# Kernel optimization log

Measured on AMD Instinct MI355X. Metric: run time of the kernel, lower is better.

Reference implementation:

```python
import jax, jax.numpy as jnp
import numpy as np

N = 250_000        # nodes
E = 8_000_000      # directed edges
F_IN = 16          # dataset.num_features
H = 8              # latent_dim
G = 512            # number of graphs in the batch


def setup_inputs() -> dict:
    key = jax.random.key(0)
    k = jax.random.split(key, 9)
    x = jax.random.normal(k[0], (N, F_IN), dtype=jnp.float32)
    edge_index = jax.random.randint(k[1], (2, E), 0, N, dtype=jnp.int64)
    batch = jnp.sort(jax.random.randint(k[2], (N,), 0, G, dtype=jnp.int64))
    W1 = jax.random.normal(k[3], (F_IN, H), dtype=jnp.float32) * 0.25
    b1 = jax.random.normal(k[4], (H,), dtype=jnp.float32) * 0.1
    W2 = jax.random.normal(k[5], (H, H), dtype=jnp.float32) * 0.35
    b2 = jax.random.normal(k[6], (H,), dtype=jnp.float32) * 0.1
    Wl = jax.random.normal(k[7], (H, 1), dtype=jnp.float32) * 0.35
    bl = jax.random.normal(k[8], (1,), dtype=jnp.float32) * 0.1
    return {"x": x, "edge_index": edge_index, "batch": batch,
            "W1": W1, "b1": b1, "W2": W2, "b2": b2, "Wl": Wl, "bl": bl}


def _gcn_conv(x, src, dst, deg_inv_sqrt, W, b, num_nodes):
    # PyG GCNConv (default): h = x @ W ; msg = norm * h[src] ; scatter-add to dst ; + bias
    h = x @ W                                    # [N, H]
    norm = deg_inv_sqrt[src] * deg_inv_sqrt[dst]  # [E+N]
    msgs = h[src] * norm[:, None]                 # [E+N, H]
    out = jax.ops.segment_sum(msgs, dst, num_segments=num_nodes)
    return out + b


def reference(x, edge_index, batch, W1, b1, W2, b2, Wl, bl):
    num_nodes = x.shape[0]
    loops = jnp.arange(num_nodes, dtype=edge_index.dtype)
    src = jnp.concatenate([edge_index[0], loops])  # self-loops appended
    dst = jnp.concatenate([edge_index[1], loops])
    # symmetric normalization: deg over destination (incl. self-loops)
    deg = jax.ops.segment_sum(jnp.ones_like(dst, dtype=x.dtype), dst,
                              num_segments=num_nodes)
    dis = jnp.where(deg > 0, jax.lax.rsqrt(jnp.maximum(deg, 1.0)), 0.0)
    h = jax.nn.relu(_gcn_conv(x, src, dst, dis, W1, b1, num_nodes))
    h = jax.nn.relu(_gcn_conv(h, src, dst, dis, W2, b2, num_nodes))
    pooled = jax.ops.segment_sum(h, batch, num_segments=G)  # global_add_pool -> [G, H]
    return jax.nn.sigmoid(pooled @ Wl + bl)                 # [G, 1]
```

## Files before the change

### kernel.cpp

```cpp
#include <hip/hip_runtime.h>
#include <math.h>

#define BLK 256
#define CH 4096
#define NBMAX 1024


__global__ void k_init0(int* __restrict__ ghist, float* __restrict__ zacc,
                        int* __restrict__ rowptr, int nb, int ng, int n, int E,
                        int primary) {
  int i = blockIdx.x * BLK + threadIdx.x;
  if (i < nb) ghist[i] = 0;
  if (i < ng) zacc[i] = 0.f;
  if (primary && i == 0) rowptr[n] = E;
}

__global__ void k_hist(const int* __restrict__ dst, int* __restrict__ ghist,
                       int E, int nb, int chunk) {
  __shared__ int h[NBMAX];
  for (int i = threadIdx.x; i < NBMAX; i += BLK) h[i] = 0;
  __syncthreads();
  long long s0 = (long long)blockIdx.x * chunk;
  int c = (int)min((long long)chunk, (long long)E - s0);
  if (c == chunk && (chunk & 3) == 0) {
    const int4* d4 = (const int4*)(dst + s0);
    int m = chunk >> 2;
    for (int i = threadIdx.x; i < m; i += BLK) {
      int4 v = d4[i];
      atomicAdd(&h[v.x >> 8], 1); atomicAdd(&h[v.y >> 8], 1);
      atomicAdd(&h[v.z >> 8], 1); atomicAdd(&h[v.w >> 8], 1);
    }
  } else {
    for (int i = threadIdx.x; i < c; i += BLK)
      atomicAdd(&h[dst[s0 + i] >> 8], 1);
  }
  __syncthreads();
  for (int b = threadIdx.x; b < nb; b += BLK)
    if (h[b]) atomicAdd(&ghist[b], h[b]);
}

__global__ void k_scan(const int* __restrict__ ghist, int* __restrict__ base,
                       int* __restrict__ cursor, int nb, int E) {
  __shared__ int temp[BLK];
  int t = threadIdx.x;
  int v[4]; int sm = 0;
  #pragma unroll
  for (int k = 0; k < 4; ++k) {
    int idx = t * 4 + k;
    v[k] = (idx < nb) ? ghist[idx] : 0;
    sm += v[k];
  }
  temp[t] = sm; __syncthreads();
  int inc = sm;
  for (int off = 1; off < BLK; off <<= 1) {
    int u = (t >= off) ? temp[t - off] : 0; __syncthreads();
    inc += u; temp[t] = inc; __syncthreads();
  }
  int run = inc - sm;
  #pragma unroll
  for (int k = 0; k < 4; ++k) {
    int idx = t * 4 + k;
    if (idx < nb) { base[idx] = run; cursor[idx] = run; }
    run += v[k];
  }
  if (t == BLK - 1) base[nb] = E;
}

__global__ void k_bin(const int* __restrict__ src, const int* __restrict__ dst,
                      int* __restrict__ cursor, int* __restrict__ binned,
                      int E, int nb) {
  __shared__ int cb[NBMAX + 1];
  __shared__ int cur[NBMAX];
  __shared__ int gofs[NBMAX];
  __shared__ int temp[BLK];
  __shared__ int stage[CH];
  __shared__ unsigned short bkt[CH];
  int t = threadIdx.x;
  for (int i = t; i < NBMAX; i += BLK) { cb[i] = 0; cur[i] = 0; }
  __syncthreads();
  long long s0 = (long long)blockIdx.x * CH;
  int c = (int)min((long long)CH, (long long)E - s0);
  if (c == CH) {
    const int4* d4 = (const int4*)(dst + s0);
    for (int i = t; i < (CH >> 2); i += BLK) {
      int4 v = d4[i];
      atomicAdd(&cb[v.x >> 8], 1); atomicAdd(&cb[v.y >> 8], 1);
      atomicAdd(&cb[v.z >> 8], 1); atomicAdd(&cb[v.w >> 8], 1);
    }
  } else {
    for (int i = t; i < c; i += BLK) atomicAdd(&cb[dst[s0 + i] >> 8], 1);
  }
  __syncthreads();
  int v[4];
  #pragma unroll
  for (int k = 0; k < 4; ++k) v[k] = cb[t * 4 + k];
  int sm = v[0] + v[1] + v[2] + v[3];
  temp[t] = sm; __syncthreads();
  int inc = sm;
  for (int off = 1; off < BLK; off <<= 1) {
    int u = (t >= off) ? temp[t - off] : 0; __syncthreads();
    inc += u; temp[t] = inc; __syncthreads();
  }
  #pragma unroll
  for (int k = 0; k < 4; ++k) {
    int b = t * 4 + k;
    if (v[k]) gofs[b] = atomicAdd(&cursor[b], v[k]);
  }
  int run = inc - sm;
  #pragma unroll
  for (int k = 0; k < 4; ++k) { cb[t * 4 + k] = run; run += v[k]; }
  if (t == BLK - 1) cb[NBMAX] = c;
  __syncthreads();
  #pragma unroll
  for (int k = 0; k < 4; ++k) {
    int b = t * 4 + k;
    int s_ = cb[b], e_ = cb[b + 1];
    if (e_ > s_) {
      gofs[b] -= s_;
      for (int i = s_; i < e_; ++i) bkt[i] = (unsigned short)b;
    }
  }
  __syncthreads();
  if (c == CH) {
    const int4* d4 = (const int4*)(dst + s0);
    const int4* s4 = (const int4*)(src + s0);
    for (int i = t; i < (CH >> 2); i += BLK) {
      int4 dv = d4[i]; int4 sv = s4[i];
      int b, r;
      b = dv.x >> 8; r = atomicAdd(&cur[b], 1); stage[cb[b] + r] = (sv.x << 8) | (dv.x & 255);
      b = dv.y >> 8; r = atomicAdd(&cur[b], 1); stage[cb[b] + r] = (sv.y << 8) | (dv.y & 255);
      b = dv.z >> 8; r = atomicAdd(&cur[b], 1); stage[cb[b] + r] = (sv.z << 8) | (dv.z & 255);
      b = dv.w >> 8; r = atomicAdd(&cur[b], 1); stage[cb[b] + r] = (sv.w << 8) | (dv.w & 255);
    }
  } else {
    for (int i = t; i < c; i += BLK) {
      int d = dst[s0 + i];
      int b = d >> 8;
      int r = atomicAdd(&cur[b], 1);
      stage[cb[b] + r] = (src[s0 + i] << 8) | (d & 255);
    }
  }
  __syncthreads();
  for (int i = t; i < c; i += BLK) {
    int b = bkt[i];
    binned[(size_t)i + gofs[b]] = stage[i];
  }
}

__global__ void k_sortdis(const int* __restrict__ base, const int* __restrict__ binned,
                          int* __restrict__ csr, int* __restrict__ rowptr,
                          float* __restrict__ dis, int n) {
  __shared__ int cnt[256], loff[256], cur[256], temp[BLK];
  int b = blockIdx.x, t = threadIdx.x;
  cnt[t] = 0; cur[t] = 0;
  __syncthreads();
  int s = base[b], e = base[b + 1];
  for (int i = s + t; i < e; i += BLK) atomicAdd(&cnt[binned[i] & 255], 1);
  __syncthreads();
  int v = cnt[t];
  temp[t] = v; __syncthreads();
  int inc = v;
  for (int off = 1; off < BLK; off <<= 1) {
    int u = (t >= off) ? temp[t - off] : 0; __syncthreads();
    inc += u; temp[t] = inc; __syncthreads();
  }
  loff[t] = inc - v;
  int node = b * 256 + t;
  if (node < n) {
    rowptr[node] = s + inc - v;
    dis[node] = rsqrtf((float)(v + 1));
  }
  __syncthreads();
  for (int i = s + t; i < e; i += BLK) {
    int rec = binned[i];
    int L = rec & 255;
    int p = atomicAdd(&cur[L], 1);
    csr[s + loff[L] + p] = rec >> 8;
  }
}

__global__ void k_gmid(const int* __restrict__ rowptr, const int* __restrict__ csr,
                       const float* __restrict__ y, float* __restrict__ y2,
                       const float* __restrict__ dis, const float* __restrict__ W2,
                       const float* __restrict__ b1, int n) {
  __shared__ float sW[64], sb[8];
  if (threadIdx.x < 64) sW[threadIdx.x] = W2[threadIdx.x];
  if (threadIdx.x < 8)  sb[threadIdx.x] = b1[threadIdx.x];
  __syncthreads();
  int node = (int)(((long long)blockIdx.x * BLK + threadIdx.x) >> 6);
  if (node >= n) return;
  int lane = threadIdx.x & 63;
  int e = lane & 31, fq = lane >> 5;
  int start = rowptr[node], end = rowptr[node + 1];
  float4 s = make_float4(0.f, 0.f, 0.f, 0.f);
  int k = start + e;
  int sidx = (k < end) ? csr[k] : -1;
  for (int k0 = start; k0 < end; k0 += 32) {
    int nk = k0 + 32 + e;
    int nsidx = (nk < end) ? csr[nk] : -1;
    if (sidx >= 0) {
      const float4 v = *(const float4*)(y + (size_t)sidx * 8 + fq * 4);
      s.x += v.x; s.y += v.y; s.z += v.z; s.w += v.w;
    }
    sidx = nsidx;
  }
  #pragma unroll
  for (int m = 1; m <= 16; m <<= 1) {
    s.x += __shfl_xor(s.x, m);
    s.y += __shfl_xor(s.y, m);
    s.z += __shfl_xor(s.z, m);
    s.w += __shfl_xor(s.w, m);
  }
  float h0 = __shfl(s.x, lane | 32);
  float h1 = __shfl(s.y, lane | 32);
  float h2 = __shfl(s.z, lane | 32);
  float h3 = __shfl(s.w, lane | 32);
  int j = lane;
  float accj = (j == 0) ? s.x : (j == 1) ? s.y : (j == 2) ? s.z : (j == 3) ? s.w
             : (j == 4) ? h0  : (j == 5) ? h1  : (j == 6) ? h2  : h3;
  float dsv = dis[node];
  float yj = (lane < 8) ? y[(size_t)node * 8 + lane] : 0.f;
  float bj = (lane < 8) ? sb[lane] : 0.f;
  float hv = fmaxf(fmaf(dsv, accj + yj, bj), 0.f);
  float o = 0.f;
  #pragma unroll
  for (int kk = 0; kk < 8; ++kk) {
    float hk = __shfl(hv, kk);
    if (lane < 8) o = fmaf(hk, sW[kk * 8 + lane], o);
  }
  if (lane < 8) y2[(size_t)node * 8 + lane] = dsv * o;
}

__global__ void k_gfin(const int* __restrict__ rowptr, const int* __restrict__ csr,
                       const float* __restrict__ y2, const float* __restrict__ dis,
                       const float* __restrict__ b2, const float* __restrict__ Wl,
                       float* __restrict__ zn, int n) {
  __shared__ float sb[8], sw[8];
  if (threadIdx.x < 8) { sb[threadIdx.x] = b2[threadIdx.x]; sw[threadIdx.x] = Wl[threadIdx.x]; }
  __syncthreads();
  int node = (int)(((long long)blockIdx.x * BLK + threadIdx.x) >> 6);
  if (node >= n) return;
  int lane = threadIdx.x & 63;
  int e = lane & 31, fq = lane >> 5;
  int start = rowptr[node], end = rowptr[node + 1];
  float4 s = make_float4(0.f, 0.f, 0.f, 0.f);
  int k = start + e;
  int sidx = (k < end) ? csr[k] : -1;
  for (int k0 = start; k0 < end; k0 += 32) {
    int nk = k0 + 32 + e;
    int nsidx = (nk < end) ? csr[nk] : -1;
    if (sidx >= 0) {
      const float4 v = *(const float4*)(y2 + (size_t)sidx * 8 + fq * 4);
      s.x += v.x; s.y += v.y; s.z += v.z; s.w += v.w;
    }
    sidx = nsidx;
  }
  #pragma unroll
  for (int m = 1; m <= 16; m <<= 1) {
    s.x += __shfl_xor(s.x, m);
    s.y += __shfl_xor(s.y, m);
    s.z += __shfl_xor(s.z, m);
    s.w += __shfl_xor(s.w, m);
  }
  float h0 = __shfl(s.x, lane | 32);
  float h1 = __shfl(s.y, lane | 32);
  float h2 = __shfl(s.z, lane | 32);
  float h3 = __shfl(s.w, lane | 32);
  int j = lane;
  float accj = (j == 0) ? s.x : (j == 1) ? s.y : (j == 2) ? s.z : (j == 3) ? s.w
             : (j == 4) ? h0  : (j == 5) ? h1  : (j == 6) ? h2  : h3;
  float dsv = dis[node];
  float yj = (lane < 8) ? y2[(size_t)node * 8 + lane] : 0.f;
  float bj = (lane < 8) ? sb[lane] : 0.f;
  float wj = (lane < 8) ? sw[lane] : 0.f;
  float p = fmaxf(fmaf(dsv, accj + yj, bj), 0.f) * wj;
  p += __shfl_xor(p, 1);
  p += __shfl_xor(p, 2);
  p += __shfl_xor(p, 4);
  if (lane == 0) zn[node] = p;
}

__global__ void k_pool(const float* __restrict__ zn, const int* __restrict__ batch,
                       float* __restrict__ zacc, int n) {
  int i = blockIdx.x * BLK + threadIdx.x;
  float s = 0.f;
  int g = -1;
  if (i < n) { s = zn[i]; g = batch[i]; }
  int g0 = __shfl(g, 0);
  bool uni = __all(g == g0);
  if (uni) {
    #pragma unroll
    for (int off = 32; off > 0; off >>= 1) s += __shfl_down(s, off);
    if ((threadIdx.x & 63) == 0 && g0 >= 0) unsafeAtomicAdd(&zacc[g0], s);
  } else if (i < n) {
    unsafeAtomicAdd(&zacc[g], s);
  }
}


__global__ void k_degdis(const int* __restrict__ base, const int* __restrict__ binned,
                         float* __restrict__ dis, int n) {
  __shared__ int deg[256];
  int b = blockIdx.x, t = threadIdx.x;
  deg[t] = 1;
  __syncthreads();
  int s = base[b], e = base[b + 1];
  for (int i = s + t; i < e; i += BLK) atomicAdd(&deg[binned[i] & 255], 1);
  __syncthreads();
  int node = b * 256 + t;
  if (node < n) dis[node] = rsqrtf((float)deg[t]);
}

__global__ void k_acc(const int* __restrict__ base, const int* __restrict__ binned,
                      const float* __restrict__ y, float* __restrict__ acc, int n) {
  __shared__ float fa[2048];
  int b = blockIdx.x, t = threadIdx.x;
  for (int i = t; i < 2048; i += BLK) fa[i] = 0.f;
  __syncthreads();
  int s = base[b], e = base[b + 1];
  int j = t & 7;
  for (int i = s + (t >> 3); i < e; i += 32) {
    int rec = binned[i];
    atomicAdd(&fa[(rec & 255) * 8 + j], y[(size_t)(rec >> 8) * 8 + j]);
  }
  __syncthreads();
  int node0 = b * 256;
  int lim = (n - node0 < 256 ? n - node0 : 256) * 8;
  for (int i = t; i < lim; i += BLK) acc[(size_t)node0 * 8 + i] = fa[i];
}


__global__ void k_y1n(const float* __restrict__ x, const float* __restrict__ W1,
                      const float* __restrict__ dis, float* __restrict__ y, int n) {
  __shared__ float sW[128];
  if (threadIdx.x < 128) sW[threadIdx.x] = W1[threadIdx.x];
  __syncthreads();
  int i = blockIdx.x * BLK + threadIdx.x;
  if (i >= n) return;
  const float4* xp = (const float4*)(x + (size_t)i * 16);
  float4 a = xp[0], bb = xp[1], cc = xp[2], d4 = xp[3];
  float xv[16] = {a.x,a.y,a.z,a.w, bb.x,bb.y,bb.z,bb.w,
                  cc.x,cc.y,cc.z,cc.w, d4.x,d4.y,d4.z,d4.w};
  float ds = dis[i];
  float o[8];
  #pragma unroll
  for (int jj = 0; jj < 8; ++jj) {
    float s = 0.f;
    #pragma unroll
    for (int k = 0; k < 16; ++k) s = fmaf(xv[k], sW[k*8 + jj], s);
    o[jj] = ds * s;
  }
  float4* yp = (float4*)(y + (size_t)i * 8);
  yp[0] = make_float4(o[0], o[1], o[2], o[3]);
  yp[1] = make_float4(o[4], o[5], o[6], o[7]);
}

__global__ void k_mid(const float* __restrict__ dis, float* __restrict__ y,
                      float* __restrict__ acc, const float* __restrict__ W2,
                      const float* __restrict__ b1, int n, int zero_acc) {
  __shared__ float sW[64];
  __shared__ float sb[8];
  if (threadIdx.x < 64) sW[threadIdx.x] = W2[threadIdx.x];
  if (threadIdx.x < 8)  sb[threadIdx.x] = b1[threadIdx.x];
  __syncthreads();
  int i = blockIdx.x * BLK + threadIdx.x;
  if (i >= n) return;
  float d = dis[i];
  float4* yp = (float4*)(y + (size_t)i * 8);
  float4* ap = (float4*)(acc + (size_t)i * 8);
  float4 y0 = yp[0], y1v = yp[1], a0 = ap[0], a1 = ap[1];
  float yy[8] = {y0.x,y0.y,y0.z,y0.w, y1v.x,y1v.y,y1v.z,y1v.w};
  float aa[8] = {a0.x,a0.y,a0.z,a0.w, a1.x,a1.y,a1.z,a1.w};
  float hv[8];
  #pragma unroll
  for (int jj = 0; jj < 8; ++jj) hv[jj] = fmaxf(fmaf(d, yy[jj] + aa[jj], sb[jj]), 0.f);
  float o[8];
  #pragma unroll
  for (int jj = 0; jj < 8; ++jj) {
    float s = 0.f;
    #pragma unroll
    for (int k = 0; k < 8; ++k) s = fmaf(hv[k], sW[k*8 + jj], s);
    o[jj] = d * s;
  }
  yp[0] = make_float4(o[0], o[1], o[2], o[3]);
  yp[1] = make_float4(o[4], o[5], o[6], o[7]);
  if (zero_acc) {
    ap[0] = make_float4(0.f, 0.f, 0.f, 0.f);
    ap[1] = make_float4(0.f, 0.f, 0.f, 0.f);
  }
}

__global__ void k_final(const float* __restrict__ dis, const float* __restrict__ y,
                        const float* __restrict__ acc, const float* __restrict__ b2,
                        const float* __restrict__ Wl, const int* __restrict__ batch,
                        float* __restrict__ zacc, int n) {
  __shared__ float sb[8], sw[8];
  if (threadIdx.x < 8) { sb[threadIdx.x] = b2[threadIdx.x]; sw[threadIdx.x] = Wl[threadIdx.x]; }
  __syncthreads();
  int i = blockIdx.x * BLK + threadIdx.x;
  float s = 0.f;
  int g = -1;
  if (i < n) {
    float d = dis[i];
    const float4* yp = (const float4*)(y + (size_t)i * 8);
    const float4* ap = (const float4*)(acc + (size_t)i * 8);
    float4 y0 = yp[0], y1v = yp[1], a0 = ap[0], a1 = ap[1];
    float yy[8] = {y0.x,y0.y,y0.z,y0.w, y1v.x,y1v.y,y1v.z,y1v.w};
    float aa[8] = {a0.x,a0.y,a0.z,a0.w, a1.x,a1.y,a1.z,a1.w};
    #pragma unroll
    for (int jj = 0; jj < 8; ++jj) {
      float h = fmaxf(fmaf(d, yy[jj] + aa[jj], sb[jj]), 0.f);
      s = fmaf(h, sw[jj], s);
    }
    g = batch[i];
  }
  int g0 = __shfl(g, 0);
  bool uni = __all(g == g0);
  if (uni) {
    #pragma unroll
    for (int off = 32; off > 0; off >>= 1) s += __shfl_down(s, off);
    if ((threadIdx.x & 63) == 0 && g0 >= 0) unsafeAtomicAdd(&zacc[g0], s);
  } else if (i < n) {
    unsafeAtomicAdd(&zacc[g], s);
  }
}

__global__ void k_out(const float* __restrict__ zacc, const float* __restrict__ bl,
                      float* __restrict__ out, int ng) {
  int i = blockIdx.x * BLK + threadIdx.x;
  if (i < ng) {
    float z = zacc[i] + bl[0];
    float r;
    if (z >= 0.f) { r = 1.f / (1.f + expf(-z)); }
    else          { float e = expf(z); r = e / (1.f + e); }
    out[i] = r;
  }
}


__global__ void k_init(int* __restrict__ deg, float* __restrict__ acc,
                       float* __restrict__ zacc, int n, int accn, int ng) {
  int jj = blockIdx.x * BLK + threadIdx.x;
  if (jj < accn) acc[jj] = 0.f;
  if (jj < n) deg[jj] = 1;
  if (jj < ng) zacc[jj] = 0.f;
}

__global__ void k_deg(const int* __restrict__ dst, int* __restrict__ deg, int E) {
  int i = blockIdx.x * BLK + threadIdx.x;
  if (i < E) atomicAdd(&deg[dst[i]], 1);
}

__global__ void k_y1(const float* __restrict__ x, const float* __restrict__ W1,
                     int* __restrict__ degdis, float* __restrict__ y, int n) {
  __shared__ float sW[128];
  if (threadIdx.x < 128) sW[threadIdx.x] = W1[threadIdx.x];
  __syncthreads();
  int i = blockIdx.x * BLK + threadIdx.x;
  if (i >= n) return;
  const float4* xp = (const float4*)(x + (size_t)i * 16);
  float4 a = xp[0], bb = xp[1], cc = xp[2], d4 = xp[3];
  float xv[16] = {a.x,a.y,a.z,a.w, bb.x,bb.y,bb.z,bb.w,
                  cc.x,cc.y,cc.z,cc.w, d4.x,d4.y,d4.z,d4.w};
  float ds = rsqrtf((float)degdis[i]);
  float o[8];
  #pragma unroll
  for (int jj = 0; jj < 8; ++jj) {
    float s = 0.f;
    #pragma unroll
    for (int k = 0; k < 16; ++k) s = fmaf(xv[k], sW[k*8 + jj], s);
    o[jj] = ds * s;
  }
  ((float*)degdis)[i] = ds;
  float4* yp = (float4*)(y + (size_t)i * 8);
  yp[0] = make_float4(o[0], o[1], o[2], o[3]);
  yp[1] = make_float4(o[4], o[5], o[6], o[7]);
}

__global__ void k_scatter(const int* __restrict__ src, const int* __restrict__ dst,
                          const float* __restrict__ y, float* __restrict__ acc,
                          long long total) {
  long long t = (long long)blockIdx.x * BLK + threadIdx.x;
  if (t >= total) return;
  int e = (int)(t >> 3);
  int h = (int)(t & 7);
  int s = src[e], d = dst[e];
  unsafeAtomicAdd(&acc[(size_t)d * 8 + h], y[(size_t)s * 8 + h]);
}


static inline size_t alignup(size_t v) { return (v + 255) & ~(size_t)255; }

extern "C" void kernel_launch(void* const* d_in, const int* in_sizes, int n_in,
                              void* d_out, int out_size, void* d_ws, size_t ws_size,
                              hipStream_t stream) {
  const float* x   = (const float*)d_in[0];
  const int*   ei  = (const int*)  d_in[1];
  const int*   bat = (const int*)  d_in[2];
  const float* W1  = (const float*)d_in[3];
  const float* b1  = (const float*)d_in[4];
  const float* W2  = (const float*)d_in[5];
  const float* b2  = (const float*)d_in[6];
  const float* Wl  = (const float*)d_in[7];
  const float* bl  = (const float*)d_in[8];
  float* out = (float*)d_out;

  int n  = in_sizes[0] / 16;
  int E  = in_sizes[1] / 2;
  int ng = out_size;

  const int* src = ei;
  const int* dst = ei + E;

  int nb = (n + 255) >> 8;

  char* wsb = (char*)d_ws;
  size_t offY  = alignup((size_t)n * 4);
  size_t offA  = offY + alignup((size_t)n * 8 * 4);
  size_t offZ  = offA + alignup((size_t)n * 8 * 4);
  size_t offZn = offZ + alignup((size_t)ng * 4);
  size_t offH  = offZn + alignup((size_t)n * 4);
  size_t offB  = offH + alignup((size_t)NBMAX * 4);
  size_t offCu = offB + alignup((size_t)(NBMAX + 1) * 4);
  size_t offBn = offCu + alignup((size_t)NBMAX * 4);
  size_t offRp = offBn + alignup((size_t)E * 4);
  size_t offCs = offRp + alignup(((size_t)n + 1) * 4);
  size_t need1 = offCs + alignup((size_t)E * 4);
  size_t need2 = offRp;

  float* dis    = (float*)wsb;
  int*   deg    = (int*)wsb;
  float* y      = (float*)(wsb + offY);
  float* acc    = (float*)(wsb + offA);
  float* zacc   = (float*)(wsb + offZ);
  float* zn     = (float*)(wsb + offZn);
  int*   ghist  = (int*)(wsb + offH);
  int*   base   = (int*)(wsb + offB);
  int*   cursor = (int*)(wsb + offCu);
  int*   binned = (int*)(wsb + offBn);
  int*   rowptr = (int*)(wsb + offRp);
  int*   csr    = (int*)(wsb + offCs);

  int gN = (n + BLK - 1) / BLK;
  int gG = (ng + BLK - 1) / BLK;
  int gW = (int)(((long long)n * 64 + BLK - 1) / BLK);

  bool ok_bin = (nb <= NBMAX) && (n < (1 << 23));
  bool tier1 = ok_bin && (ws_size >= need1);
  bool tier2 = ok_bin && (ws_size >= need2);

  if (tier1 || tier2) {
    int histChunk = 8192;
    int gHist = (int)(((long long)E + histChunk - 1) / histChunk);
    int gBin  = (int)(((long long)E + CH - 1) / CH);
    int gI0   = (NBMAX > ng ? NBMAX : ng) / BLK + 1;
    k_init0 <<<gI0, BLK, 0, stream>>>(ghist, zacc, rowptr, NBMAX, ng, n, E, tier1 ? 1 : 0);
    k_hist  <<<gHist, BLK, 0, stream>>>(dst, ghist, E, nb, histChunk);
    k_scan  <<<1, BLK, 0, stream>>>(ghist, base, cursor, nb, E);
    k_bin   <<<gBin, BLK, 0, stream>>>(src, dst, cursor, binned, E, nb);
    if (tier1) {
      k_sortdis<<<nb, BLK, 0, stream>>>(base, binned, csr, rowptr, dis, n);
      k_y1n   <<<gN, BLK, 0, stream>>>(x, W1, dis, y, n);
      k_gmid  <<<gW, BLK, 0, stream>>>(rowptr, csr, y, acc, dis, W2, b1, n);
      k_gfin  <<<gW, BLK, 0, stream>>>(rowptr, csr, acc, dis, b2, Wl, zn, n);
      k_pool  <<<gN, BLK, 0, stream>>>(zn, bat, zacc, n);
    } else {
      k_degdis<<<nb, BLK, 0, stream>>>(base, binned, dis, n);
      k_y1n   <<<gN, BLK, 0, stream>>>(x, W1, dis, y, n);
      k_acc   <<<nb, BLK, 0, stream>>>(base, binned, y, acc, n);
      k_mid   <<<gN, BLK, 0, stream>>>(dis, y, acc, W2, b1, n, 0);
      k_acc   <<<nb, BLK, 0, stream>>>(base, binned, y, acc, n);
      k_final <<<gN, BLK, 0, stream>>>(dis, y, acc, b2, Wl, bat, zacc, n);
    }
  } else {
    int accn = n * 8;
    long long tot = (long long)E * 8;
    int gInit = (accn + BLK - 1) / BLK;
    int gE    = (E + BLK - 1) / BLK;
    int gS    = (int)((tot + BLK - 1) / BLK);
    k_init   <<<gInit, BLK, 0, stream>>>(deg, acc, zacc, n, accn, ng);
    k_deg    <<<gE, BLK, 0, stream>>>(dst, deg, E);
    k_y1     <<<gN, BLK, 0, stream>>>(x, W1, deg, y, n);
    k_scatter<<<gS, BLK, 0, stream>>>(src, dst, y, acc, tot);
    k_mid    <<<gN, BLK, 0, stream>>>(dis, y, acc, W2, b1, n, 1);
    k_scatter<<<gS, BLK, 0, stream>>>(src, dst, y, acc, tot);
    k_final  <<<gN, BLK, 0, stream>>>(dis, y, acc, b2, Wl, bat, zacc, n);
  }
  k_out<<<gG, BLK, 0, stream>>>(zacc, bl, out, ng);
}
```

Measured before the change: 548.4 us.

## Store node features in bf16 for CSR gathers and simplify edge binning

Intermediate per-node features y and y2 are now stored as bf16, which halves the bytes gathered per edge in the two CSR aggregation kernels. The binning kernel drops its vectorized int4 paths and per-slot bucket array, and instead finds each staged element's bucket by binary search over the bucket offsets. The tier2 fallback path and its kernels are removed. This adds bf16 rounding error to the aggregated features, and the binning kernel does more work per element in exchange for less shared memory.

```diff
diff --git a/kernel.cpp b/kernel.cpp
--- a/kernel.cpp
+++ b/kernel.cpp
@@ -4,6 +4,16 @@
 #define BLK 256
 #define CH 4096
 #define NBMAX 1024
+
+typedef unsigned short ushortT;
+
+__device__ __forceinline__ float bf2f(unsigned short u) {
+  return __uint_as_float(((unsigned int)u) << 16);
+}
+__device__ __forceinline__ unsigned short f2bf(float f) {
+  unsigned int u = __float_as_uint(f);
+  return (unsigned short)((u + 0x7fffu + ((u >> 16) & 1u)) >> 16);
+}
 
 
 __global__ void k_init0(int* __restrict__ ghist, float* __restrict__ zacc,
@@ -69,81 +79,43 @@
 __global__ void k_bin(const int* __restrict__ src, const int* __restrict__ dst,
                       int* __restrict__ cursor, int* __restrict__ binned,
                       int E, int nb) {
-  __shared__ int cb[NBMAX + 1];
-  __shared__ int cur[NBMAX];
-  __shared__ int gofs[NBMAX];
-  __shared__ int temp[BLK];
+  __shared__ int cnt[NBMAX], cur[NBMAX], gofs[NBMAX], baseA[NBMAX + 1], temp[BLK];
   __shared__ int stage[CH];
-  __shared__ unsigned short bkt[CH];
   int t = threadIdx.x;
-  for (int i = t; i < NBMAX; i += BLK) { cb[i] = 0; cur[i] = 0; }
+  for (int i = t; i < NBMAX; i += BLK) { cnt[i] = 0; cur[i] = 0; }
   __syncthreads();
   long long s0 = (long long)blockIdx.x * CH;
   int c = (int)min((long long)CH, (long long)E - s0);
-  if (c == CH) {
-    const int4* d4 = (const int4*)(dst + s0);
-    for (int i = t; i < (CH >> 2); i += BLK) {
-      int4 v = d4[i];
-      atomicAdd(&cb[v.x >> 8], 1); atomicAdd(&cb[v.y >> 8], 1);
-      atomicAdd(&cb[v.z >> 8], 1); atomicAdd(&cb[v.w >> 8], 1);
-    }
-  } else {
-    for (int i = t; i < c; i += BLK) atomicAdd(&cb[dst[s0 + i] >> 8], 1);
-  }
-  __syncthreads();
-  int v[4];
-  #pragma unroll
-  for (int k = 0; k < 4; ++k) v[k] = cb[t * 4 + k];
-  int sm = v[0] + v[1] + v[2] + v[3];
+  for (int i = t; i < c; i += BLK) atomicAdd(&cnt[dst[s0 + i] >> 8], 1);
+  __syncthreads();
+  int v[4], sm = 0;
+  #pragma unroll
+  for (int k = 0; k < 4; ++k) { v[k] = cnt[t * 4 + k]; sm += v[k]; }
   temp[t] = sm; __syncthreads();
   int inc = sm;
   for (int off = 1; off < BLK; off <<= 1) {
     int u = (t >= off) ? temp[t - off] : 0; __syncthreads();
     inc += u; temp[t] = inc; __syncthreads();
   }
-  #pragma unroll
-  for (int k = 0; k < 4; ++k) {
-    int b = t * 4 + k;
-    if (v[k]) gofs[b] = atomicAdd(&cursor[b], v[k]);
-  }
   int run = inc - sm;
   #pragma unroll
-  for (int k = 0; k < 4; ++k) { cb[t * 4 + k] = run; run += v[k]; }
-  if (t == BLK - 1) cb[NBMAX] = c;
-  __syncthreads();
-  #pragma unroll
-  for (int k = 0; k < 4; ++k) {
-    int b = t * 4 + k;
-    int s_ = cb[b], e_ = cb[b + 1];
-    if (e_ > s_) {
-      gofs[b] -= s_;
-      for (int i = s_; i < e_; ++i) bkt[i] = (unsigned short)b;
-    }
-  }
-  __syncthreads();
-  if (c == CH) {
-    const int4* d4 = (const int4*)(dst + s0);
-    const int4* s4 = (const int4*)(src + s0);
-    for (int i = t; i < (CH >> 2); i += BLK) {
-      int4 dv = d4[i]; int4 sv = s4[i];
-      int b, r;
-      b = dv.x >> 8; r = atomicAdd(&cur[b], 1); stage[cb[b] + r] = (sv.x << 8) | (dv.x & 255);
-      b = dv.y >> 8; r = atomicAdd(&cur[b], 1); stage[cb[b] + r] = (sv.y << 8) | (dv.y & 255);
-      b = dv.z >> 8; r = atomicAdd(&cur[b], 1); stage[cb[b] + r] = (sv.z << 8) | (dv.z & 255);
-      b = dv.w >> 8; r = atomicAdd(&cur[b], 1); stage[cb[b] + r] = (sv.w << 8) | (dv.w & 255);
-    }
-  } else {
-    for (int i = t; i < c; i += BLK) {
-      int d = dst[s0 + i];
-      int b = d >> 8;
-      int r = atomicAdd(&cur[b], 1);
-      stage[cb[b] + r] = (src[s0 + i] << 8) | (d & 255);
-    }
-  }
+  for (int k = 0; k < 4; ++k) { baseA[t * 4 + k] = run; run += v[k]; }
+  if (t == BLK - 1) baseA[NBMAX] = c;
+  __syncthreads();
+  for (int b = t; b < nb; b += BLK)
+    if (cnt[b]) gofs[b] = atomicAdd(&cursor[b], cnt[b]);
   __syncthreads();
   for (int i = t; i < c; i += BLK) {
-    int b = bkt[i];
-    binned[(size_t)i + gofs[b]] = stage[i];
+    int d = dst[s0 + i];
+    int b = d >> 8;
+    int r = atomicAdd(&cur[b], 1);
+    stage[baseA[b] + r] = (src[s0 + i] << 8) | (d & 255);
+  }
+  __syncthreads();
+  for (int i = t; i < c; i += BLK) {
+    int lo = 0, hi = nb;
+    while (hi - lo > 1) { int m = (lo + hi) >> 1; if (baseA[m] <= i) lo = m; else hi = m; }
+    binned[(size_t)gofs[lo] + (i - baseA[lo])] = stage[i];
   }
 }
 
@@ -179,8 +151,36 @@
   }
 }
 
+__global__ void k_y1b(const float* __restrict__ x, const float* __restrict__ W1,
+                      const float* __restrict__ dis, ushortT* __restrict__ ybf, int n) {
+  __shared__ float sW[128];
+  if (threadIdx.x < 128) sW[threadIdx.x] = W1[threadIdx.x];
+  __syncthreads();
+  int i = blockIdx.x * BLK + threadIdx.x;
+  if (i >= n) return;
+  const float4* xp = (const float4*)(x + (size_t)i * 16);
+  float4 a = xp[0], bb = xp[1], cc = xp[2], d4 = xp[3];
+  float xv[16] = {a.x,a.y,a.z,a.w, bb.x,bb.y,bb.z,bb.w,
+                  cc.x,cc.y,cc.z,cc.w, d4.x,d4.y,d4.z,d4.w};
+  float ds = dis[i];
+  float o[8];
+  #pragma unroll
+  for (int jj = 0; jj < 8; ++jj) {
+    float s = 0.f;
+    #pragma unroll
+    for (int k = 0; k < 16; ++k) s = fmaf(xv[k], sW[k*8 + jj], s);
+    o[jj] = ds * s;
+  }
+  uint4 p;
+  p.x = (unsigned int)f2bf(o[0]) | ((unsigned int)f2bf(o[1]) << 16);
+  p.y = (unsigned int)f2bf(o[2]) | ((unsigned int)f2bf(o[3]) << 16);
+  p.z = (unsigned int)f2bf(o[4]) | ((unsigned int)f2bf(o[5]) << 16);
+  p.w = (unsigned int)f2bf(o[6]) | ((unsigned int)f2bf(o[7]) << 16);
+  *(uint4*)(ybf + (size_t)i * 8) = p;
+}
+
 __global__ void k_gmid(const int* __restrict__ rowptr, const int* __restrict__ csr,
-                       const float* __restrict__ y, float* __restrict__ y2,
+                       const ushortT* __restrict__ ybf, ushortT* __restrict__ y2bf,
                        const float* __restrict__ dis, const float* __restrict__ W2,
                        const float* __restrict__ b1, int n) {
   __shared__ float sW[64], sb[8];
@@ -199,8 +199,11 @@
     int nk = k0 + 32 + e;
     int nsidx = (nk < end) ? csr[nk] : -1;
     if (sidx >= 0) {
-      const float4 v = *(const float4*)(y + (size_t)sidx * 8 + fq * 4);
-      s.x += v.x; s.y += v.y; s.z += v.z; s.w += v.w;
+      const uint2 v = *(const uint2*)(ybf + (size_t)sidx * 8 + fq * 4);
+      s.x += __uint_as_float(v.x << 16);
+      s.y += __uint_as_float(v.x & 0xFFFF0000u);
+      s.z += __uint_as_float(v.y << 16);
+      s.w += __uint_as_float(v.y & 0xFFFF0000u);
     }
     sidx = nsidx;
   }
@@ -219,7 +222,7 @@
   float accj = (j == 0) ? s.x : (j == 1) ? s.y : (j == 2) ? s.z : (j == 3) ? s.w
              : (j == 4) ? h0  : (j == 5) ? h1  : (j == 6) ? h2  : h3;
   float dsv = dis[node];
-  float yj = (lane < 8) ? y[(size_t)node * 8 + lane] : 0.f;
+  float yj = (lane < 8) ? bf2f(ybf[(size_t)node * 8 + lane]) : 0.f;
   float bj = (lane < 8) ? sb[lane] : 0.f;
   float hv = fmaxf(fmaf(dsv, accj + yj, bj), 0.f);
   float o = 0.f;
@@ -228,11 +231,11 @@
     float hk = __shfl(hv, kk);
     if (lane < 8) o = fmaf(hk, sW[kk * 8 + lane], o);
   }
-  if (lane < 8) y2[(size_t)node * 8 + lane] = dsv * o;
+  if (lane < 8) y2bf[(size_t)node * 8 + lane] = f2bf(dsv * o);
 }
 
 __global__ void k_gfin(const int* __restrict__ rowptr, const int* __restrict__ csr,
-                       const float* __restrict__ y2, const float* __restrict__ dis,
+                       const ushortT* __restrict__ y2bf, const float* __restrict__ dis,
                        const float* __restrict__ b2, const float* __restrict__ Wl,
                        float* __restrict__ zn, int n) {
   __shared__ float sb[8], sw[8];
@@ -250,8 +253,11 @@
     int nk = k0 + 32 + e;
     int nsidx = (nk < end) ? csr[nk] : -1;
     if (sidx >= 0) {
-      const float4 v = *(const float4*)(y2 + (size_t)sidx * 8 + fq * 4);
-      s.x += v.x; s.y += v.y; s.z += v.z; s.w += v.w;
+      const uint2 v = *(const uint2*)(y2bf + (size_t)sidx * 8 + fq * 4);
+      s.x += __uint_as_float(v.x << 16);
+      s.y += __uint_as_float(v.x & 0xFFFF0000u);
+      s.z += __uint_as_float(v.y << 16);
+      s.w += __uint_as_float(v.y & 0xFFFF0000u);
     }
     sidx = nsidx;
   }
@@ -270,7 +276,7 @@
   float accj = (j == 0) ? s.x : (j == 1) ? s.y : (j == 2) ? s.z : (j == 3) ? s.w
              : (j == 4) ? h0  : (j == 5) ? h1  : (j == 6) ? h2  : h3;
   float dsv = dis[node];
-  float yj = (lane < 8) ? y2[(size_t)node * 8 + lane] : 0.f;
+  float yj = (lane < 8) ? bf2f(y2bf[(size_t)node * 8 + lane]) : 0.f;
   float bj = (lane < 8) ? sb[lane] : 0.f;
   float wj = (lane < 8) ? sw[lane] : 0.f;
   float p = fmaxf(fmaf(dsv, accj + yj, bj), 0.f) * wj;
@@ -297,41 +303,34 @@
   }
 }
 
-
-__global__ void k_degdis(const int* __restrict__ base, const int* __restrict__ binned,
-                         float* __restrict__ dis, int n) {
-  __shared__ int deg[256];
-  int b = blockIdx.x, t = threadIdx.x;
-  deg[t] = 1;
-  __syncthreads();
-  int s = base[b], e = base[b + 1];
-  for (int i = s + t; i < e; i += BLK) atomicAdd(&deg[binned[i] & 255], 1);
-  __syncthreads();
-  int node = b * 256 + t;
-  if (node < n) dis[node] = rsqrtf((float)deg[t]);
-}
-
-__global__ void k_acc(const int* __restrict__ base, const int* __restrict__ binned,
-                      const float* __restrict__ y, float* __restrict__ acc, int n) {
-  __shared__ float fa[2048];
-  int b = blockIdx.x, t = threadIdx.x;
-  for (int i = t; i < 2048; i += BLK) fa[i] = 0.f;
-  __syncthreads();
-  int s = base[b], e = base[b + 1];
-  int j = t & 7;
-  for (int i = s + (t >> 3); i < e; i += 32) {
-    int rec = binned[i];
-    atomicAdd(&fa[(rec & 255) * 8 + j], y[(size_t)(rec >> 8) * 8 + j]);
-  }
-  __syncthreads();
-  int node0 = b * 256;
-  int lim = (n - node0 < 256 ? n - node0 : 256) * 8;
-  for (int i = t; i < lim; i += BLK) acc[(size_t)node0 * 8 + i] = fa[i];
-}
-
-
-__global__ void k_y1n(const float* __restrict__ x, const float* __restrict__ W1,
-                      const float* __restrict__ dis, float* __restrict__ y, int n) {
+__global__ void k_out(const float* __restrict__ zacc, const float* __restrict__ bl,
+                      float* __restrict__ out, int ng) {
+  int i = blockIdx.x * BLK + threadIdx.x;
+  if (i < ng) {
+    float z = zacc[i] + bl[0];
+    float r;
+    if (z >= 0.f) { r = 1.f / (1.f + expf(-z)); }
+    else          { float e = expf(z); r = e / (1.f + e); }
+    out[i] = r;
+  }
+}
+
+
+__global__ void k_init(int* __restrict__ deg, float* __restrict__ acc,
+                       float* __restrict__ zacc, int n, int accn, int ng) {
+  int jj = blockIdx.x * BLK + threadIdx.x;
+  if (jj < accn) acc[jj] = 0.f;
+  if (jj < n) deg[jj] = 1;
+  if (jj < ng) zacc[jj] = 0.f;
+}
+
+__global__ void k_deg(const int* __restrict__ dst, int* __restrict__ deg, int E) {
+  int i = blockIdx.x * BLK + threadIdx.x;
+  if (i < E) atomicAdd(&deg[dst[i]], 1);
+}
+
+__global__ void k_y1(const float* __restrict__ x, const float* __restrict__ W1,
+                     int* __restrict__ degdis, float* __restrict__ y, int n) {
   __shared__ float sW[128];
   if (threadIdx.x < 128) sW[threadIdx.x] = W1[threadIdx.x];
   __syncthreads();
@@ -341,7 +340,7 @@
   float4 a = xp[0], bb = xp[1], cc = xp[2], d4 = xp[3];
   float xv[16] = {a.x,a.y,a.z,a.w, bb.x,bb.y,bb.z,bb.w,
                   cc.x,cc.y,cc.z,cc.w, d4.x,d4.y,d4.z,d4.w};
-  float ds = dis[i];
+  float ds = rsqrtf((float)degdis[i]);
   float o[8];
   #pragma unroll
   for (int jj = 0; jj < 8; ++jj) {
@@ -350,9 +349,21 @@
     for (int k = 0; k < 16; ++k) s = fmaf(xv[k], sW[k*8 + jj], s);
     o[jj] = ds * s;
   }
+  ((float*)degdis)[i] = ds;
   float4* yp = (float4*)(y + (size_t)i * 8);
   yp[0] = make_float4(o[0], o[1], o[2], o[3]);
   yp[1] = make_float4(o[4], o[5], o[6], o[7]);
+}
+
+__global__ void k_scatter(const int* __restrict__ src, const int* __restrict__ dst,
+                          const float* __restrict__ y, float* __restrict__ acc,
+                          long long total) {
+  long long t = (long long)blockIdx.x * BLK + threadIdx.x;
+  if (t >= total) return;
+  int e = (int)(t >> 3);
+  int h = (int)(t & 7);
+  int s = src[e], d = dst[e];
+  unsafeAtomicAdd(&acc[(size_t)d * 8 + h], y[(size_t)s * 8 + h]);
 }
 
 __global__ void k_mid(const float* __restrict__ dis, float* __restrict__ y,
@@ -425,69 +436,6 @@
   }
 }
 
-__global__ void k_out(const float* __restrict__ zacc, const float* __restrict__ bl,
-                      float* __restrict__ out, int ng) {
-  int i = blockIdx.x * BLK + threadIdx.x;
-  if (i < ng) {
-    float z = zacc[i] + bl[0];
-    float r;
-    if (z >= 0.f) { r = 1.f / (1.f + expf(-z)); }
-    else          { float e = expf(z); r = e / (1.f + e); }
-    out[i] = r;
-  }
-}
-
-
-__global__ void k_init(int* __restrict__ deg, float* __restrict__ acc,
-                       float* __restrict__ zacc, int n, int accn, int ng) {
-  int jj = blockIdx.x * BLK + threadIdx.x;
-  if (jj < accn) acc[jj] = 0.f;
-  if (jj < n) deg[jj] = 1;
-  if (jj < ng) zacc[jj] = 0.f;
-}
-
-__global__ void k_deg(const int* __restrict__ dst, int* __restrict__ deg, int E) {
-  int i = blockIdx.x * BLK + threadIdx.x;
-  if (i < E) atomicAdd(&deg[dst[i]], 1);
-}
-
-__global__ void k_y1(const float* __restrict__ x, const float* __restrict__ W1,
-                     int* __restrict__ degdis, float* __restrict__ y, int n) {
-  __shared__ float sW[128];
-  if (threadIdx.x < 128) sW[threadIdx.x] = W1[threadIdx.x];
-  __syncthreads();
-  int i = blockIdx.x * BLK + threadIdx.x;
-  if (i >= n) return;
-  const float4* xp = (const float4*)(x + (size_t)i * 16);
-  float4 a = xp[0], bb = xp[1], cc = xp[2], d4 = xp[3];
-  float xv[16] = {a.x,a.y,a.z,a.w, bb.x,bb.y,bb.z,bb.w,
-                  cc.x,cc.y,cc.z,cc.w, d4.x,d4.y,d4.z,d4.w};
-  float ds = rsqrtf((float)degdis[i]);
-  float o[8];
-  #pragma unroll
-  for (int jj = 0; jj < 8; ++jj) {
-    float s = 0.f;
-    #pragma unroll
-    for (int k = 0; k < 16; ++k) s = fmaf(xv[k], sW[k*8 + jj], s);
-    o[jj] = ds * s;
-  }
-  ((float*)degdis)[i] = ds;
-  float4* yp = (float4*)(y + (size_t)i * 8);
-  yp[0] = make_float4(o[0], o[1], o[2], o[3]);
-  yp[1] = make_float4(o[4], o[5], o[6], o[7]);
-}
-
-__global__ void k_scatter(const int* __restrict__ src, const int* __restrict__ dst,
-                          const float* __restrict__ y, float* __restrict__ acc,
-                          long long total) {
-  long long t = (long long)blockIdx.x * BLK + threadIdx.x;
-  if (t >= total) return;
-  int e = (int)(t >> 3);
-  int h = (int)(t & 7);
-  int s = src[e], d = dst[e];
-  unsafeAtomicAdd(&acc[(size_t)d * 8 + h], y[(size_t)s * 8 + h]);
-}
-
 
 static inline size_t alignup(size_t v) { return (v + 255) & ~(size_t)255; }
 
@@ -526,20 +474,21 @@
   size_t offRp = offBn + alignup((size_t)E * 4);
   size_t offCs = offRp + alignup(((size_t)n + 1) * 4);
   size_t need1 = offCs + alignup((size_t)E * 4);
-  size_t need2 = offRp;
-
-  float* dis    = (float*)wsb;
-  int*   deg    = (int*)wsb;
-  float* y      = (float*)(wsb + offY);
-  float* acc    = (float*)(wsb + offA);
-  float* zacc   = (float*)(wsb + offZ);
-  float* zn     = (float*)(wsb + offZn);
-  int*   ghist  = (int*)(wsb + offH);
-  int*   base   = (int*)(wsb + offB);
-  int*   cursor = (int*)(wsb + offCu);
-  int*   binned = (int*)(wsb + offBn);
-  int*   rowptr = (int*)(wsb + offRp);
-  int*   csr    = (int*)(wsb + offCs);
+
+  float*   dis    = (float*)wsb;
+  int*     deg    = (int*)wsb;
+  float*   y      = (float*)(wsb + offY);
+  ushortT* ybf    = (ushortT*)(wsb + offY);
+  float*   acc    = (float*)(wsb + offA);
+  ushortT* y2bf   = (ushortT*)(wsb + offA);
+  float*   zacc   = (float*)(wsb + offZ);
+  float*   zn     = (float*)(wsb + offZn);
+  int*     ghist  = (int*)(wsb + offH);
+  int*     base   = (int*)(wsb + offB);
+  int*     cursor = (int*)(wsb + offCu);
+  int*     binned = (int*)(wsb + offBn);
+  int*     rowptr = (int*)(wsb + offRp);
+  int*     csr    = (int*)(wsb + offCs);
 
   int gN = (n + BLK - 1) / BLK;
   int gG = (ng + BLK - 1) / BLK;
@@ -547,31 +496,21 @@
 
   bool ok_bin = (nb <= NBMAX) && (n < (1 << 23));
   bool tier1 = ok_bin && (ws_size >= need1);
-  bool tier2 = ok_bin && (ws_size >= need2);
-
-  if (tier1 || tier2) {
+
+  if (tier1) {
     int histChunk = 8192;
     int gHist = (int)(((long long)E + histChunk - 1) / histChunk);
     int gBin  = (int)(((long long)E + CH - 1) / CH);
     int gI0   = (NBMAX > ng ? NBMAX : ng) / BLK + 1;
-    k_init0 <<<gI0, BLK, 0, stream>>>(ghist, zacc, rowptr, NBMAX, ng, n, E, tier1 ? 1 : 0);
+    k_init0 <<<gI0, BLK, 0, stream>>>(ghist, zacc, rowptr, NBMAX, ng, n, E, 1);
     k_hist  <<<gHist, BLK, 0, stream>>>(dst, ghist, E, nb, histChunk);
     k_scan  <<<1, BLK, 0, stream>>>(ghist, base, cursor, nb, E);
     k_bin   <<<gBin, BLK, 0, stream>>>(src, dst, cursor, binned, E, nb);
-    if (tier1) {
-      k_sortdis<<<nb, BLK, 0, stream>>>(base, binned, csr, rowptr, dis, n);
-      k_y1n   <<<gN, BLK, 0, stream>>>(x, W1, dis, y, n);
-      k_gmid  <<<gW, BLK, 0, stream>>>(rowptr, csr, y, acc, dis, W2, b1, n);
-      k_gfin  <<<gW, BLK, 0, stream>>>(rowptr, csr, acc, dis, b2, Wl, zn, n);
-      k_pool  <<<gN, BLK, 0, stream>>>(zn, bat, zacc, n);
-    } else {
-      k_degdis<<<nb, BLK, 0, stream>>>(base, binned, dis, n);
-      k_y1n   <<<gN, BLK, 0, stream>>>(x, W1, dis, y, n);
-      k_acc   <<<nb, BLK, 0, stream>>>(base, binned, y, acc, n);
-      k_mid   <<<gN, BLK, 0, stream>>>(dis, y, acc, W2, b1, n, 0);
-      k_acc   <<<nb, BLK, 0, stream>>>(base, binned, y, acc, n);
-      k_final <<<gN, BLK, 0, stream>>>(dis, y, acc, b2, Wl, bat, zacc, n);
-    }
+    k_sortdis<<<nb, BLK, 0, stream>>>(base, binned, csr, rowptr, dis, n);
+    k_y1b   <<<gN, BLK, 0, stream>>>(x, W1, dis, ybf, n);
+    k_gmid  <<<gW, BLK, 0, stream>>>(rowptr, csr, ybf, y2bf, dis, W2, b1, n);
+    k_gfin  <<<gW, BLK, 0, stream>>>(rowptr, csr, y2bf, dis, b2, Wl, zn, n);
+    k_pool  <<<gN, BLK, 0, stream>>>(zn, bat, zacc, n);
   } else {
     int accn = n * 8;
     long long tot = (long long)E * 8;
```

New measurement: 459.9 us. 16.1% less time.
